# Kernel tuning notes

Measured on AMD Instinct MI355X. Metric: run time of the kernel, lower is better.

Reference implementation:

```python
import jax, jax.numpy as jnp
import numpy as np

NEG = -1.0e30  # safe stand-in for -inf (avoids nan in gradients)
EPS = 1e-7     # keras.backend.epsilon()


def _ctc_loss(true_labels, true_lengths, y_pred, input_lengths):
    """CTC negative log-likelihood, matching keras.backend.ctc_batch_cost.

    true_labels:   [B, L] int labels (blank = V-1 excluded)
    true_lengths:  [B, 1] label lengths
    y_pred:        [B, T, V] softmax probabilities
    input_lengths: [B, 1] number of valid time frames
    returns:       [B, 1] loss
    """
    B, T, V = y_pred.shape
    L = true_labels.shape[1]
    S = 2 * L + 1
    blank = V - 1

    logp = jnp.log(y_pred + EPS)                                   # [B,T,V]

    # Extended label sequence: blank, l1, blank, l2, ..., blank
    ext = jnp.full((B, S), blank, dtype=true_labels.dtype)
    ext = ext.at[:, 1::2].set(true_labels)                          # [B,S]
    ext_m2 = jnp.concatenate(
        [jnp.full((B, 2), blank, dtype=ext.dtype), ext[:, :-2]], axis=1)
    s_idx = jnp.arange(S)
    can_skip = (s_idx >= 2)[None, :] & (ext != blank) & (ext != ext_m2)  # [B,S]

    # Per-extended-position log-probs at every time step: [B,T,S]
    lp_ext = jax.vmap(lambda lp_b, e_b: lp_b[:, e_b])(logp, ext)

    def step(alpha, inp):
        t, lp_t = inp                                               # lp_t [B,S]
        a1 = jnp.concatenate([jnp.full((B, 1), NEG), alpha[:, :-1]], axis=1)
        a2 = jnp.concatenate([jnp.full((B, 2), NEG), alpha[:, :-2]], axis=1)
        m = jnp.logaddexp(alpha, a1)
        m = jnp.where(can_skip, jnp.logaddexp(m, a2), m)
        new = m + lp_t
        # freeze alpha for sequences past their input length
        new = jnp.where(t < input_lengths, new, alpha)              # [B,1] bcast
        return new, None

    # alpha_{-1}: probability 1 at a virtual start before position 0
    alpha0 = jnp.full((B, S), NEG).at[:, 0].set(0.0)
    alpha, _ = jax.lax.scan(
        step, alpha0, (jnp.arange(T), jnp.transpose(lp_ext, (1, 0, 2))))

    lab = true_lengths[:, 0]
    b_idx = jnp.arange(B)
    a_last = alpha[b_idx, 2 * lab]          # ends at final blank
    a_prev = alpha[b_idx, 2 * lab - 1]      # ends at final label
    return -jnp.logaddexp(a_last, a_prev)[:, None]                  # [B,1]


def setup_inputs() -> dict:
    key = jax.random.key(0)
    k1, k2, k3 = jax.random.split(key, 3)
    B, T, V, L = 128, 1024, 512, 128
    logits = jax.random.normal(k1, (B, T, V), dtype=jnp.float32)
    predicted_labels = jax.nn.softmax(logits, axis=-1)              # probabilities
    true_labels = jax.random.randint(k2, (B, L), 0, V - 1)          # exclude blank
    true_lengths = jax.random.randint(k3, (B, 1), 16, L + 1)
    predicted_lengths = jnp.full((B, 1), T, dtype=jnp.int32)
    return {
        "true_labels": true_labels,
        "true_lengths": true_lengths,
        "predicted_labels": predicted_labels,
        "predicted_lengths": predicted_lengths,
    }


def reference(true_labels, true_lengths, predicted_labels, predicted_lengths):
    # CTCLayer.call returns predicted_labels and registers the loss via
    # add_loss; the computation of interest is the CTC loss itself.
    return _ctc_loss(true_labels, true_lengths, predicted_labels, predicted_lengths)
```

## Files before the change

### kernel.cpp

```cpp
#include <hip/hip_runtime.h>

constexpr int Tc = 1024;
constexpr int Vc = 512;
constexpr int Lc = 128;
constexpr int Sc = 2 * Lc + 1;
constexpr int BLANK = Vc - 1;
constexpr float NEGF = -1e30f;
constexpr float EPSF = 1e-7f;
constexpr int PF = 16;

__device__ __forceinline__ float lae2(float x, float y) {
    float m = fmaxf(x, y);
    return m + __logf(__expf(x - m) + __expf(y - m));
}
__device__ __forceinline__ float lae3(float x, float y, float z) {
    float m = fmaxf(fmaxf(x, y), z);
    return m + __logf(__expf(x - m) + __expf(y - m) + __expf(z - m));
}

__launch_bounds__(64, 1)
__global__ void ctc_fwd_wave(const int* __restrict__ labels,
                             const int* __restrict__ label_len,
                             const float* __restrict__ probs,
                             const int* __restrict__ input_len,
                             float* __restrict__ out)
{
    const int b    = blockIdx.x;
    const int lane = threadIdx.x;

    __shared__ float sa[Sc];

    const int lbase = b * Lc;
    const int l0  = labels[lbase + 2 * lane];
    const int l1  = labels[lbase + 2 * lane + 1];
    const int lm1 = (lane > 0) ? labels[lbase + 2 * lane - 1] : 0;
    const bool cs1 = (lane > 0) && (l0 != lm1);
    const bool cs3 = (l1 != l0);
    const int len = input_len[b];

    const float* __restrict__ base = probs + (size_t)b * Tc * Vc;
    const float* __restrict__ pB = base + BLANK;
    const float* __restrict__ p1 = base + l0;
    const float* __restrict__ p2 = base + l1;

#define RING16(X) X(0) X(1) X(2) X(3) X(4) X(5) X(6) X(7) \
                  X(8) X(9) X(10) X(11) X(12) X(13) X(14) X(15)
#define DECLR(j) float rb##j, r1##j, r2##j;
    RING16(DECLR)
#undef DECLR
#define INITR(j) { const size_t o = (size_t)(j) * Vc; \
                   rb##j = pB[o]; r1##j = p1[o]; r2##j = p2[o]; }
    RING16(INITR)
#undef INITR

    float a0 = (lane == 0) ? 0.0f : NEGF;
    float a1 = NEGF;
    float a2 = NEGF;
    float a3 = NEGF;
    float a4 = NEGF;
    float u3 = NEGF;

#define STEP(t, j, REFILL) { \
        const float lpb = __logf(rb##j + EPSF); \
        const float lp1 = __logf(r1##j + EPSF); \
        const float lp2 = __logf(r2##j + EPSF); \
        if (REFILL) { const size_t o = (size_t)((t) + PF) * Vc; \
            rb##j = pB[o]; r1##j = p1[o]; r2##j = p2[o]; } \
        const float n3 = lae3(a3, a2, cs3 ? a1 : NEGF) + lp2; \
        const float u3n = __shfl_up(n3, 1); \
        const float n0 = lae2(a0, u3) + lpb; \
        const float n1 = lae3(a1, a0, cs1 ? u3 : NEGF) + lp1; \
        const float n2 = lae2(a2, a1) + lpb; \
        const float n4 = lae2(a4, a3) + lpb; \
        const bool live = ((t) < len); \
        a0 = live ? n0 : a0; \
        a1 = live ? n1 : a1; \
        a2 = live ? n2 : a2; \
        a3 = live ? n3 : a3; \
        a4 = live ? n4 : a4; \
        u3 = live ? ((lane == 0) ? NEGF : u3n) : u3; \
    }

#define STEPS16(t0, R) \
        STEP((t0)+0,  0,  R) STEP((t0)+1,  1,  R) STEP((t0)+2,  2,  R) STEP((t0)+3,  3,  R) \
        STEP((t0)+4,  4,  R) STEP((t0)+5,  5,  R) STEP((t0)+6,  6,  R) STEP((t0)+7,  7,  R) \
        STEP((t0)+8,  8,  R) STEP((t0)+9,  9,  R) STEP((t0)+10, 10, R) STEP((t0)+11, 11, R) \
        STEP((t0)+12, 12, R) STEP((t0)+13, 13, R) STEP((t0)+14, 14, R) STEP((t0)+15, 15, R)

    for (int t0 = 0; t0 < Tc - PF; t0 += PF) {
        STEPS16(t0, 1)
    }
    STEPS16(Tc - PF, 0)

#undef STEP
#undef STEPS16
#undef RING16

    sa[4 * lane + 0] = a0;
    sa[4 * lane + 1] = a1;
    sa[4 * lane + 2] = a2;
    sa[4 * lane + 3] = a3;
    if (lane == 63) sa[256] = a4;
    __syncthreads();
    if (lane == 0) {
        const int lab = label_len[b];
        const float x = sa[2 * lab];
        const float y = sa[2 * lab - 1];
        out[b] = -lae2(x, y);
    }
}

extern "C" void kernel_launch(void* const* d_in, const int* in_sizes, int n_in,
                              void* d_out, int out_size, void* d_ws, size_t ws_size,
                              hipStream_t stream) {
    const int*   labels    = (const int*)d_in[0];
    const int*   label_len = (const int*)d_in[1];
    const float* probs     = (const float*)d_in[2];
    const int*   input_len = (const int*)d_in[3];
    float*       out       = (float*)d_out;

    const int B = in_sizes[1];
    ctc_fwd_wave<<<B, 64, 0, stream>>>(labels, label_len, probs, input_len, out);
}
```

Baseline: 696.6 us.

## Stream full probability rows into LDS ring via async global_load_lds DMA

Measured after the change: 662.6 us. 1.05x faster.

```diff
diff --git a/kernel.cpp b/kernel.cpp
--- a/kernel.cpp
+++ b/kernel.cpp
@@ -7,7 +7,7 @@
 constexpr int BLANK = Vc - 1;
 constexpr float NEGF = -1e30f;
 constexpr float EPSF = 1e-7f;
-constexpr int PF = 16;
+constexpr int RING = 16;
 
 __device__ __forceinline__ float lae2(float x, float y) {
     float m = fmaxf(x, y);
@@ -28,6 +28,7 @@
     const int b    = blockIdx.x;
     const int lane = threadIdx.x;
 
+    __shared__ float rows[RING][Vc];
     __shared__ float sa[Sc];
 
     const int lbase = b * Lc;
@@ -38,20 +39,40 @@
     const bool cs3 = (l1 != l0);
     const int len = input_len[b];
 
-    const float* __restrict__ base = probs + (size_t)b * Tc * Vc;
-    const float* __restrict__ pB = base + BLANK;
-    const float* __restrict__ p1 = base + l0;
-    const float* __restrict__ p2 = base + l1;
+    const float* __restrict__ srow = probs + (size_t)b * Tc * Vc;
+    const float* __restrict__ gl   = srow + lane * 4;
 
-#define RING16(X) X(0) X(1) X(2) X(3) X(4) X(5) X(6) X(7) \
-                  X(8) X(9) X(10) X(11) X(12) X(13) X(14) X(15)
-#define DECLR(j) float rb##j, r1##j, r2##j;
-    RING16(DECLR)
-#undef DECLR
-#define INITR(j) { const size_t o = (size_t)(j) * Vc; \
-                   rb##j = pB[o]; r1##j = p1[o]; r2##j = p2[o]; }
-    RING16(INITR)
-#undef INITR
+    const unsigned ldsRows = (unsigned)(size_t)&rows[0][0];
+    const unsigned cB = ldsRows + (unsigned)(BLANK * 4);
+    const unsigned c1 = ldsRows + (unsigned)l0 * 4u;
+    const unsigned c2 = ldsRows + (unsigned)l1 * 4u;
+
+    asm volatile("" :: "v"(lm1), "v"(len));
+    asm volatile("s_waitcnt vmcnt(0) lgkmcnt(0)" ::: "memory");
+
+#define DMA_ROW(slot, trow) do { \
+        const float* gp_ = gl + (size_t)(trow) * Vc; \
+        __builtin_amdgcn_global_load_lds( \
+            (const __attribute__((address_space(1))) void*)(size_t)gp_, \
+            (__attribute__((address_space(3))) void*)(size_t)(ldsRows + (unsigned)((slot) * (Vc * 4))), \
+            16, 0, 0); \
+        __builtin_amdgcn_global_load_lds( \
+            (const __attribute__((address_space(1))) void*)(size_t)(gp_ + 256), \
+            (__attribute__((address_space(3))) void*)(size_t)(ldsRows + (unsigned)((slot) * (Vc * 4) + 1024)), \
+            16, 0, 0); \
+    } while (0)
+
+#define DSREAD(dst, addr) asm volatile("ds_read_b32 %0, %1" : "=v"(dst) : "v"(addr))
+#define WAIT_VM(N)  asm volatile("s_waitcnt vmcnt(" #N ")" ::: "memory")
+#define WAIT_LGKM3(x, y, z) \
+    asm volatile("s_waitcnt lgkmcnt(3)" : "+v"(x), "+v"(y), "+v"(z) :: "memory")
+#define WAIT_LGKM0(x, y, z) \
+    asm volatile("s_waitcnt lgkmcnt(0)" : "+v"(x), "+v"(y), "+v"(z) :: "memory")
+
+    DMA_ROW(0, 0)  ; DMA_ROW(1, 1)  ; DMA_ROW(2, 2)  ; DMA_ROW(3, 3)  ;
+    DMA_ROW(4, 4)  ; DMA_ROW(5, 5)  ; DMA_ROW(6, 6)  ; DMA_ROW(7, 7)  ;
+    DMA_ROW(8, 8)  ; DMA_ROW(9, 9)  ; DMA_ROW(10, 10); DMA_ROW(11, 11);
+    DMA_ROW(12, 12); DMA_ROW(13, 13); DMA_ROW(14, 14); DMA_ROW(15, 15);
 
     float a0 = (lane == 0) ? 0.0f : NEGF;
     float a1 = NEGF;
@@ -60,19 +81,31 @@
     float a4 = NEGF;
     float u3 = NEGF;
 
-#define STEP(t, j, REFILL) { \
-        const float lpb = __logf(rb##j + EPSF); \
-        const float lp1 = __logf(r1##j + EPSF); \
-        const float lp2 = __logf(r2##j + EPSF); \
-        if (REFILL) { const size_t o = (size_t)((t) + PF) * Vc; \
-            rb##j = pB[o]; r1##j = p1[o]; r2##j = p2[o]; } \
+    float fAb, fA1, fA2, fBb, fB1, fB2;
+
+    WAIT_VM(30);
+    DSREAD(fAb, cB); DSREAD(fA1, c1); DSREAD(fA2, c2);
+
+#define STEP(t_, j, NV, DOB, DOD, CB_, C1_, C2_, NB_, N1_, N2_, LG) { \
+        WAIT_VM(NV); \
+        if (DOB) { \
+            const unsigned sl_ = (unsigned)((((j) + 1) & (RING - 1)) * (Vc * 4)); \
+            unsigned ab_ = cB + sl_, ax_ = c1 + sl_, ay_ = c2 + sl_; \
+            DSREAD(NB_, ab_); DSREAD(N1_, ax_); DSREAD(N2_, ay_); \
+        } \
+        LG(CB_, C1_, C2_); \
+        __builtin_amdgcn_sched_barrier(0); \
+        if (DOD) DMA_ROW((j), (t_) + RING); \
+        const float lpb = __logf(CB_ + EPSF); \
+        const float lp1 = __logf(C1_ + EPSF); \
+        const float lp2 = __logf(C2_ + EPSF); \
         const float n3 = lae3(a3, a2, cs3 ? a1 : NEGF) + lp2; \
         const float u3n = __shfl_up(n3, 1); \
         const float n0 = lae2(a0, u3) + lpb; \
         const float n1 = lae3(a1, a0, cs1 ? u3 : NEGF) + lp1; \
         const float n2 = lae2(a2, a1) + lpb; \
         const float n4 = lae2(a4, a3) + lpb; \
-        const bool live = ((t) < len); \
+        const bool live = ((t_) < len); \
         a0 = live ? n0 : a0; \
         a1 = live ? n1 : a1; \
         a2 = live ? n2 : a2; \
@@ -81,20 +114,47 @@
         u3 = live ? ((lane == 0) ? NEGF : u3n) : u3; \
     }
 
-#define STEPS16(t0, R) \
-        STEP((t0)+0,  0,  R) STEP((t0)+1,  1,  R) STEP((t0)+2,  2,  R) STEP((t0)+3,  3,  R) \
-        STEP((t0)+4,  4,  R) STEP((t0)+5,  5,  R) STEP((t0)+6,  6,  R) STEP((t0)+7,  7,  R) \
-        STEP((t0)+8,  8,  R) STEP((t0)+9,  9,  R) STEP((t0)+10, 10, R) STEP((t0)+11, 11, R) \
-        STEP((t0)+12, 12, R) STEP((t0)+13, 13, R) STEP((t0)+14, 14, R) STEP((t0)+15, 15, R)
-
-    for (int t0 = 0; t0 < Tc - PF; t0 += PF) {
-        STEPS16(t0, 1)
+    for (int t0 = 0; t0 < Tc - RING; t0 += 16) {
+        STEP(t0 + 0,  0,  28, 1, 1, fAb, fA1, fA2, fBb, fB1, fB2, WAIT_LGKM3)
+        STEP(t0 + 1,  1,  28, 1, 1, fBb, fB1, fB2, fAb, fA1, fA2, WAIT_LGKM3)
+        STEP(t0 + 2,  2,  28, 1, 1, fAb, fA1, fA2, fBb, fB1, fB2, WAIT_LGKM3)
+        STEP(t0 + 3,  3,  28, 1, 1, fBb, fB1, fB2, fAb, fA1, fA2, WAIT_LGKM3)
+        STEP(t0 + 4,  4,  28, 1, 1, fAb, fA1, fA2, fBb, fB1, fB2, WAIT_LGKM3)
+        STEP(t0 + 5,  5,  28, 1, 1, fBb, fB1, fB2, fAb, fA1, fA2, WAIT_LGKM3)
+        STEP(t0 + 6,  6,  28, 1, 1, fAb, fA1, fA2, fBb, fB1, fB2, WAIT_LGKM3)
+        STEP(t0 + 7,  7,  28, 1, 1, fBb, fB1, fB2, fAb, fA1, fA2, WAIT_LGKM3)
+        STEP(t0 + 8,  8,  28, 1, 1, fAb, fA1, fA2, fBb, fB1, fB2, WAIT_LGKM3)
+        STEP(t0 + 9,  9,  28, 1, 1, fBb, fB1, fB2, fAb, fA1, fA2, WAIT_LGKM3)
+        STEP(t0 + 10, 10, 28, 1, 1, fAb, fA1, fA2, fBb, fB1, fB2, WAIT_LGKM3)
+        STEP(t0 + 11, 11, 28, 1, 1, fBb, fB1, fB2, fAb, fA1, fA2, WAIT_LGKM3)
+        STEP(t0 + 12, 12, 28, 1, 1, fAb, fA1, fA2, fBb, fB1, fB2, WAIT_LGKM3)
+        STEP(t0 + 13, 13, 28, 1, 1, fBb, fB1, fB2, fAb, fA1, fA2, WAIT_LGKM3)
+        STEP(t0 + 14, 14, 28, 1, 1, fAb, fA1, fA2, fBb, fB1, fB2, WAIT_LGKM3)
+        STEP(t0 + 15, 15, 28, 1, 1, fBb, fB1, fB2, fAb, fA1, fA2, WAIT_LGKM3)
     }
-    STEPS16(Tc - PF, 0)
+    STEP(1008, 0,  26, 1, 0, fAb, fA1, fA2, fBb, fB1, fB2, WAIT_LGKM3)
+    STEP(1009, 1,  24, 1, 0, fBb, fB1, fB2, fAb, fA1, fA2, WAIT_LGKM3)
+    STEP(1010, 2,  22, 1, 0, fAb, fA1, fA2, fBb, fB1, fB2, WAIT_LGKM3)
+    STEP(1011, 3,  20, 1, 0, fBb, fB1, fB2, fAb, fA1, fA2, WAIT_LGKM3)
+    STEP(1012, 4,  18, 1, 0, fAb, fA1, fA2, fBb, fB1, fB2, WAIT_LGKM3)
+    STEP(1013, 5,  16, 1, 0, fBb, fB1, fB2, fAb, fA1, fA2, WAIT_LGKM3)
+    STEP(1014, 6,  14, 1, 0, fAb, fA1, fA2, fBb, fB1, fB2, WAIT_LGKM3)
+    STEP(1015, 7,  12, 1, 0, fBb, fB1, fB2, fAb, fA1, fA2, WAIT_LGKM3)
+    STEP(1016, 8,  10, 1, 0, fAb, fA1, fA2, fBb, fB1, fB2, WAIT_LGKM3)
+    STEP(1017, 9,  8,  1, 0, fBb, fB1, fB2, fAb, fA1, fA2, WAIT_LGKM3)
+    STEP(1018, 10, 6,  1, 0, fAb, fA1, fA2, fBb, fB1, fB2, WAIT_LGKM3)
+    STEP(1019, 11, 4,  1, 0, fBb, fB1, fB2, fAb, fA1, fA2, WAIT_LGKM3)
+    STEP(1020, 12, 2,  1, 0, fAb, fA1, fA2, fBb, fB1, fB2, WAIT_LGKM3)
+    STEP(1021, 13, 0,  1, 0, fBb, fB1, fB2, fAb, fA1, fA2, WAIT_LGKM3)
+    STEP(1022, 14, 0,  1, 0, fAb, fA1, fA2, fBb, fB1, fB2, WAIT_LGKM3)
+    STEP(1023, 15, 0,  0, 0, fBb, fB1, fB2, fAb, fA1, fA2, WAIT_LGKM0)
 
 #undef STEP
-#undef STEPS16
-#undef RING16
+#undef WAIT_LGKM0
+#undef WAIT_LGKM3
+#undef WAIT_VM
+#undef DSREAD
+#undef DMA_ROW
 
     sa[4 * lane + 0] = a0;
     sa[4 * lane + 1] = a1;
```
